# Optimization experiments

Hardware: AMD Instinct MI355X
Metric: run time of the kernel (lower is better)

Reference implementation:

```python
import jax, jax.numpy as jnp
import numpy as np

MAX_POS = 1024  # max_pos_embed_distance
H = 12          # num_heads
D = 768         # input_dim == hidden_dim
P = D // H      # head_dim


def setup_inputs() -> dict:
    key = jax.random.key(0)
    ks = jax.random.split(key, 8)
    s = 1.0 / np.sqrt(D)
    return {
        "x": jax.random.normal(ks[0], (8, 1024, D), dtype=jnp.float32),
        "wq": jax.random.uniform(ks[1], (D, D), jnp.float32, -s, s),
        "bq": jax.random.uniform(ks[2], (D,), jnp.float32, -s, s),
        "wk": jax.random.uniform(ks[3], (D, D), jnp.float32, -s, s),
        "bk": jax.random.uniform(ks[4], (D,), jnp.float32, -s, s),
        "wv": jax.random.uniform(ks[5], (D, D), jnp.float32, -s, s),
        "bv": jax.random.uniform(ks[6], (D,), jnp.float32, -s, s),
        "dist_emb": jax.random.normal(ks[7], (2 * MAX_POS - 1, P), dtype=jnp.float32),
    }


def reference(x, wq, bq, wk, bk, wv, bv, dist_emb):
    b, n, _ = x.shape
    factor = 1.0 / np.sqrt(P)
    # q,k,v: [b, n, h, p]
    q = (x @ wq.T + bq).reshape(b, n, H, P)
    k = (x @ wk.T + bk).reshape(b, n, H, P)
    v = (x @ wv.T + bv).reshape(b, n, H, P)
    raw = jnp.einsum('bihd,bjhd->bhij', q, k)
    # relative-key bias: pos_emb[i, r] = dist_emb[i - r + MAX_POS - 1]
    dist = jnp.arange(n)[:, None] - jnp.arange(n)[None, :]
    pos_emb = dist_emb[dist + MAX_POS - 1]           # [n, n, p]
    raw = raw + jnp.einsum('bihd,ird->bhir', q, pos_emb)
    # NOTE: original scales AFTER adding relative scores
    attn = jax.nn.softmax(raw * factor, axis=-1)
    out = jnp.einsum('bhij,bjhp->bihp', attn, v)
    return out.reshape(b, n, -1)
```

## Files before the change

### kernel.cpp

```cpp
#include <hip/hip_runtime.h>
#include <hip/hip_bf16.h>

#define NH 12
#define HD 64
#define DM 768
#define SEQ 1024
#define BATCH 8

typedef __attribute__((ext_vector_type(8))) short bf16x8;
typedef __attribute__((ext_vector_type(4))) short s16x4;
typedef __attribute__((ext_vector_type(4))) float f32x4;

__device__ __forceinline__ short f2b(float x) {
    unsigned u = __float_as_uint(x);
    u += 0x7fffu + ((u >> 16) & 1u);
    return (short)(u >> 16);
}

#define MFMA(A, B, C) __builtin_amdgcn_mfma_f32_16x16x32_bf16(A, B, C, 0, 0, 0)

__global__ __launch_bounds__(256) void cvt_f32_bf16(
    const float* __restrict__ in, short* __restrict__ out, int n4)
{
    int i = blockIdx.x * 256 + threadIdx.x;
    if (i < n4) {
        f32x4 v = *(const f32x4*)(in + 4 * (size_t)i);
        s16x4 r;
        r[0] = f2b(v[0]); r[1] = f2b(v[1]); r[2] = f2b(v[2]); r[3] = f2b(v[3]);
        *(s16x4*)(out + 4 * (size_t)i) = r;
    }
}

__global__ __launch_bounds__(512, 4) void qkv_mfma(
    const short* __restrict__ xb,
    const short* __restrict__ wqb, const float* __restrict__ bq,
    const short* __restrict__ wkb, const float* __restrict__ bk,
    const short* __restrict__ wvb, const float* __restrict__ bv,
    short* __restrict__ qb, short* __restrict__ kb, short* __restrict__ vt)
{
    __shared__ short Xl[128][72];
    __shared__ short Wl[64][72];

    const int orig = blockIdx.x;
    const int sw   = (orig & 7) * 288 + (orig >> 3);
    const int t    = sw % 36;
    const int by   = t % 12;
    const int z    = t / 12;
    const int bx   = sw / 36;

    const short* wmat = (z == 0) ? wqb : (z == 1) ? wkb : wvb;
    const float* bias = (z == 0) ? bq : (z == 1) ? bk : bv;

    const int i0   = bx * 128;
    const int col0 = by * 64;
    const int tid  = threadIdx.x;
    const int lane = tid & 63;
    const int w    = tid >> 6;
    const int lg   = lane >> 4;
    const int lc   = lane & 15;

    const int sr = tid >> 3, scx = (tid & 7) * 8;

    f32x4 acc[4] = {};
    for (int k0 = 0; k0 < DM; k0 += 64) {
        __syncthreads();
        *(bf16x8*)&Xl[sr][scx] =
            *(const bf16x8*)&xb[(size_t)(i0 + sr) * DM + k0 + scx];
        *(bf16x8*)&Xl[sr + 64][scx] =
            *(const bf16x8*)&xb[(size_t)(i0 + 64 + sr) * DM + k0 + scx];
        *(bf16x8*)&Wl[sr][scx] =
            *(const bf16x8*)&wmat[(size_t)(col0 + sr) * DM + k0 + scx];
        __syncthreads();
        #pragma unroll
        for (int kh = 0; kh < 2; ++kh) {
            const bf16x8 a = *(const bf16x8*)&Xl[w * 16 + lc][kh * 32 + lg * 8];
            #pragma unroll
            for (int n = 0; n < 4; ++n) {
                const bf16x8 bfr = *(const bf16x8*)&Wl[n * 16 + lc][kh * 32 + lg * 8];
                acc[n] = MFMA(a, bfr, acc[n]);
            }
        }
    }

    if (z < 2) {
        short* outp = (z == 0) ? qb : kb;
        #pragma unroll
        for (int n = 0; n < 4; ++n) {
            const int c = col0 + n * 16 + lc;
            const float bi = bias[c];
            #pragma unroll
            for (int rr = 0; rr < 4; ++rr) {
                const int r = i0 + w * 16 + lg * 4 + rr;
                outp[(size_t)r * DM + c] = f2b(acc[n][rr] + bi);
            }
        }
    } else {
        #pragma unroll
        for (int n = 0; n < 4; ++n) {
            const int c = col0 + n * 16 + lc;
            const int h = c >> 6, d = c & 63;
            const float bi = bias[c];
            #pragma unroll
            for (int rr = 0; rr < 4; ++rr) {
                const int r  = i0 + w * 16 + lg * 4 + rr;
                const int bb = r >> 10, j = r & 1023;
                vt[(((size_t)bb * NH + h) * HD + d) * SEQ + j] = f2b(acc[n][rr] + bi);
            }
        }
    }
}

__global__ __launch_bounds__(512, 4) void attn_flash(
    const short* __restrict__ qb, const short* __restrict__ kb,
    const short* __restrict__ vt, const short* __restrict__ deb,
    float* __restrict__ out)
{
    const int orig = blockIdx.x;
    const int sw   = (orig & 7) * 96 + (orig >> 3);
    const int bx   = sw & 7;
    const int rest = sw >> 3;
    const int h    = rest % NH;
    const int b    = rest / NH;

    const int i0   = bx * 128;
    const int tid  = threadIdx.x;
    const int lane = tid & 63;
    const int w    = tid >> 6;
    const int wR   = w * 16;
    const int lg   = lane >> 4;
    const int lc   = lane & 15;

    __shared__ short Kl[64][72];
    __shared__ short Dl[192][72];
    __shared__ short Pl[8][16][136];

    const short* qrow = qb + ((size_t)(b * SEQ + i0 + wR + lc)) * DM + h * HD;
    const bf16x8 A0 = *(const bf16x8*)(qrow + lg * 8);
    const bf16x8 A1 = *(const bf16x8*)(qrow + 32 + lg * 8);

    const short* kbase = kb + (size_t)(b * SEQ) * DM + h * HD;
    const short* vbase = vt + ((size_t)(b * NH + h) * HD) * SEQ;

    const int sr = tid >> 3, scx = (tid & 7) * 8;
    bf16x8 kreg, dreg0, dreg1, dreg2;

    auto stage_load = [&](int jc) {
        kreg = *(const bf16x8*)&kbase[(size_t)(jc + sr) * DM + scx];
        const int wb = i0 - jc + 960;
        const int r2 = min(wb + sr + 128, 2046);
        dreg0 = *(const bf16x8*)&deb[(size_t)(wb + sr) * HD + scx];
        dreg1 = *(const bf16x8*)&deb[(size_t)(wb + sr + 64) * HD + scx];
        dreg2 = *(const bf16x8*)&deb[(size_t)r2 * HD + scx];
    };
    auto stage_store = [&]() {
        *(bf16x8*)&Kl[sr][scx]       = kreg;
        *(bf16x8*)&Dl[sr][scx]       = dreg0;
        *(bf16x8*)&Dl[sr + 64][scx]  = dreg1;
        *(bf16x8*)&Dl[sr + 128][scx] = dreg2;
    };

    float m[4], l[4];
    f32x4 O0 = {0.f,0.f,0.f,0.f}, O1 = {0.f,0.f,0.f,0.f};
    f32x4 O2 = {0.f,0.f,0.f,0.f}, O3 = {0.f,0.f,0.f,0.f};
    #pragma unroll
    for (int rr = 0; rr < 4; ++rr) { m[rr] = -1e30f; l[rr] = 0.f; }

    stage_load(0);
    stage_store();
    __syncthreads();

    for (int c = 0; c < 16; ++c) {
        const int jc = c * 64;
        if (c < 15) stage_load(jc + 64);

        f32x4 T0, T1, T2, T3, T4;
        {
            f32x4 a;
            a = f32x4{0.f,0.f,0.f,0.f};
            a = MFMA(A0, *(const bf16x8*)&Dl[wR + 0*16 + lc][lg*8], a);
            T0 = MFMA(A1, *(const bf16x8*)&Dl[wR + 0*16 + lc][32 + lg*8], a);
            a = f32x4{0.f,0.f,0.f,0.f};
            a = MFMA(A0, *(const bf16x8*)&Dl[wR + 1*16 + lc][lg*8], a);
            T1 = MFMA(A1, *(const bf16x8*)&Dl[wR + 1*16 + lc][32 + lg*8], a);
            a = f32x4{0.f,0.f,0.f,0.f};
            a = MFMA(A0, *(const bf16x8*)&Dl[wR + 2*16 + lc][lg*8], a);
            T2 = MFMA(A1, *(const bf16x8*)&Dl[wR + 2*16 + lc][32 + lg*8], a);
            a = f32x4{0.f,0.f,0.f,0.f};
            a = MFMA(A0, *(const bf16x8*)&Dl[wR + 3*16 + lc][lg*8], a);
            T3 = MFMA(A1, *(const bf16x8*)&Dl[wR + 3*16 + lc][32 + lg*8], a);
            a = f32x4{0.f,0.f,0.f,0.f};
            a = MFMA(A0, *(const bf16x8*)&Dl[wR + 4*16 + lc][lg*8], a);
            T4 = MFMA(A1, *(const bf16x8*)&Dl[wR + 4*16 + lc][32 + lg*8], a);
        }

        f32x4 sv[4];
        #pragma unroll
        for (int jt = 0; jt < 4; ++jt) {
            f32x4 s = {0.f,0.f,0.f,0.f};
            s = MFMA(A0, *(const bf16x8*)&Kl[jt*16 + lc][lg*8], s);
            s = MFMA(A1, *(const bf16x8*)&Kl[jt*16 + lc][32 + lg*8], s);
            sv[jt] = s;
        }
        __syncthreads();

        float mw[4] = {-1e30f, -1e30f, -1e30f, -1e30f};
        #pragma unroll
        for (int jt = 0; jt < 4; ++jt) {
            #pragma unroll
            for (int rr = 0; rr < 4; ++rr) {
                const int loff = 63 + lg * 4 + rr - jt * 16 - lc;
                const int src  = (lane & 48) | (loff & 15);
                float c0, c1;
                if (jt == 0)      { c0 = __shfl(T3[rr], src, 64); c1 = __shfl(T4[rr], src, 64); }
                else if (jt == 1) { c0 = __shfl(T2[rr], src, 64); c1 = __shfl(T3[rr], src, 64); }
                else if (jt == 2) { c0 = __shfl(T1[rr], src, 64); c1 = __shfl(T2[rr], src, 64); }
                else              { c0 = __shfl(T0[rr], src, 64); c1 = __shfl(T1[rr], src, 64); }
                const int tlo = 3 - jt;
                float bias = ((loff >> 4) == tlo) ? c0 : c1;
                sv[jt][rr] += bias;
                mw[rr] = fmaxf(mw[rr], sv[jt][rr]);
            }
        }

        float scale[4];
        #pragma unroll
        for (int rr = 0; rr < 4; ++rr) {
            float v = mw[rr];
            v = fmaxf(v, __shfl_xor(v, 1, 64));
            v = fmaxf(v, __shfl_xor(v, 2, 64));
            v = fmaxf(v, __shfl_xor(v, 4, 64));
            v = fmaxf(v, __shfl_xor(v, 8, 64));
            const float mn = fmaxf(m[rr], v);
            scale[rr] = __expf((m[rr] - mn) * 0.125f);
            m[rr] = mn;
            float s = 0.f;
            #pragma unroll
            for (int jt = 0; jt < 4; ++jt) {
                const float p = __expf((sv[jt][rr] - mn) * 0.125f);
                Pl[w][lg * 4 + rr][jt * 16 + lc] = f2b(p);
                s += p;
            }
            s += __shfl_xor(s, 1, 64);
            s += __shfl_xor(s, 2, 64);
            s += __shfl_xor(s, 4, 64);
            s += __shfl_xor(s, 8, 64);
            l[rr] = l[rr] * scale[rr] + s;
        }

        if (c < 15) stage_store();

        #pragma unroll
        for (int rr = 0; rr < 4; ++rr) {
            O0[rr] *= scale[rr]; O1[rr] *= scale[rr];
            O2[rr] *= scale[rr]; O3[rr] *= scale[rr];
        }
        #pragma unroll
        for (int ks = 0; ks < 2; ++ks) {
            const bf16x8 Af = *(const bf16x8*)&Pl[w][lc][ks * 32 + lg * 8];
            const size_t vo = jc + ks * 32 + lg * 8;
            O0 = MFMA(Af, *(const bf16x8*)&vbase[(size_t)( 0 + lc) * SEQ + vo], O0);
            O1 = MFMA(Af, *(const bf16x8*)&vbase[(size_t)(16 + lc) * SEQ + vo], O1);
            O2 = MFMA(Af, *(const bf16x8*)&vbase[(size_t)(32 + lc) * SEQ + vo], O2);
            O3 = MFMA(Af, *(const bf16x8*)&vbase[(size_t)(48 + lc) * SEQ + vo], O3);
        }
        __syncthreads();
    }

    #pragma unroll
    for (int rr = 0; rr < 4; ++rr) {
        const size_t rowoff = ((size_t)(b * SEQ + i0 + wR + lg * 4 + rr)) * DM + h * HD;
        const float inv = 1.0f / l[rr];
        out[rowoff +  0 + lc] = O0[rr] * inv;
        out[rowoff + 16 + lc] = O1[rr] * inv;
        out[rowoff + 32 + lc] = O2[rr] * inv;
        out[rowoff + 48 + lc] = O3[rr] * inv;
    }
}

extern "C" void kernel_launch(void* const* d_in, const int* in_sizes, int n_in,
                              void* d_out, int out_size, void* d_ws, size_t ws_size,
                              hipStream_t stream) {
    const float* x  = (const float*)d_in[0];
    const float* wq = (const float*)d_in[1];
    const float* bq = (const float*)d_in[2];
    const float* wk = (const float*)d_in[3];
    const float* bk = (const float*)d_in[4];
    const float* wv = (const float*)d_in[5];
    const float* bv = (const float*)d_in[6];
    const float* de = (const float*)d_in[7];
    float* out = (float*)d_out;

    const size_t NX = (size_t)BATCH * SEQ * DM;
    const size_t NW = (size_t)DM * DM;
    const size_t ND = 2047 * HD;
    short* xb  = (short*)d_ws;
    short* wqb = xb  + NX;
    short* wkb = wqb + NW;
    short* wvb = wkb + NW;
    short* deb = wvb + NW;
    short* qbw = deb + ND;
    short* kbw = qbw + NX;
    short* vtw = kbw + NX;

    cvt_f32_bf16<<<(int)((NX / 4 + 255) / 256), 256, 0, stream>>>(x,  xb,  (int)(NX / 4));
    cvt_f32_bf16<<<(int)((NW / 4 + 255) / 256), 256, 0, stream>>>(wq, wqb, (int)(NW / 4));
    cvt_f32_bf16<<<(int)((NW / 4 + 255) / 256), 256, 0, stream>>>(wk, wkb, (int)(NW / 4));
    cvt_f32_bf16<<<(int)((NW / 4 + 255) / 256), 256, 0, stream>>>(wv, wvb, (int)(NW / 4));
    cvt_f32_bf16<<<(int)((ND / 4 + 255) / 256), 256, 0, stream>>>(de, deb, (int)(ND / 4));

    qkv_mfma<<<2304, 512, 0, stream>>>(xb, wqb, bq, wkb, bk, wvb, bv,
                                       qbw, kbw, vtw);
    attn_flash<<<768, 512, 0, stream>>>(qbw, kbw, vtw, deb, out);
}
```

Baseline: 383.4 us.

## Double-buffer LDS tiles in QKV and attention kernels, route bias via LDS

The QKV projection kernel now double-buffers its X/W shared tiles, so each k-step needs one barrier instead of two, and its launch-bounds occupancy hint drops from 4 to 2. The attention kernel double-buffers K tiles and drops the shared distance-embedding tile. Each wave instead reads dist_emb directly from global memory, writes the relative-position products to a per-wave float LDS buffer, and gathers the bias from there instead of using cross-lane shuffles. The P tile is XOR-swizzled to reduce LDS bank conflicts. This removes block barriers and shuffle work, at the cost of more LDS traffic, uncoalesced global loads of dist_emb and possibly lower occupancy.

```diff
diff --git a/kernel.cpp b/kernel.cpp
--- a/kernel.cpp
+++ b/kernel.cpp
@@ -18,6 +18,8 @@
 }
 
 #define MFMA(A, B, C) __builtin_amdgcn_mfma_f32_16x16x32_bf16(A, B, C, 0, 0, 0)
+
+#define PSWZ(row, col) ((col) ^ (((row) & 7) << 3))
 
 __global__ __launch_bounds__(256) void cvt_f32_bf16(
     const float* __restrict__ in, short* __restrict__ out, int n4)
@@ -31,15 +33,15 @@
     }
 }
 
-__global__ __launch_bounds__(512, 4) void qkv_mfma(
+__global__ __launch_bounds__(512, 2) void qkv_mfma(
     const short* __restrict__ xb,
     const short* __restrict__ wqb, const float* __restrict__ bq,
     const short* __restrict__ wkb, const float* __restrict__ bk,
     const short* __restrict__ wvb, const float* __restrict__ bv,
     short* __restrict__ qb, short* __restrict__ kb, short* __restrict__ vt)
 {
-    __shared__ short Xl[128][72];
-    __shared__ short Wl[64][72];
+    __shared__ short Xl[2][128][72];
+    __shared__ short Wl[2][64][72];
 
     const int orig = blockIdx.x;
     const int sw   = (orig & 7) * 288 + (orig >> 3);
@@ -61,25 +63,32 @@
 
     const int sr = tid >> 3, scx = (tid & 7) * 8;
 
+    auto stage = [&](int k0, int buf) {
+        *(bf16x8*)&Xl[buf][sr][scx] =
+            *(const bf16x8*)&xb[(size_t)(i0 + sr) * DM + k0 + scx];
+        *(bf16x8*)&Xl[buf][sr + 64][scx] =
+            *(const bf16x8*)&xb[(size_t)(i0 + 64 + sr) * DM + k0 + scx];
+        *(bf16x8*)&Wl[buf][sr][scx] =
+            *(const bf16x8*)&wmat[(size_t)(col0 + sr) * DM + k0 + scx];
+    };
+
     f32x4 acc[4] = {};
-    for (int k0 = 0; k0 < DM; k0 += 64) {
+    stage(0, 0);
+    __syncthreads();
+
+    for (int ks = 0; ks < 12; ++ks) {
+        const int cur = ks & 1;
+        if (ks < 11) stage((ks + 1) * 64, cur ^ 1);
+        #pragma unroll
+        for (int kh = 0; kh < 2; ++kh) {
+            const bf16x8 a = *(const bf16x8*)&Xl[cur][w * 16 + lc][kh * 32 + lg * 8];
+            #pragma unroll
+            for (int n = 0; n < 4; ++n) {
+                const bf16x8 bfr = *(const bf16x8*)&Wl[cur][n * 16 + lc][kh * 32 + lg * 8];
+                acc[n] = MFMA(a, bfr, acc[n]);
+            }
+        }
         __syncthreads();
-        *(bf16x8*)&Xl[sr][scx] =
-            *(const bf16x8*)&xb[(size_t)(i0 + sr) * DM + k0 + scx];
-        *(bf16x8*)&Xl[sr + 64][scx] =
-            *(const bf16x8*)&xb[(size_t)(i0 + 64 + sr) * DM + k0 + scx];
-        *(bf16x8*)&Wl[sr][scx] =
-            *(const bf16x8*)&wmat[(size_t)(col0 + sr) * DM + k0 + scx];
-        __syncthreads();
-        #pragma unroll
-        for (int kh = 0; kh < 2; ++kh) {
-            const bf16x8 a = *(const bf16x8*)&Xl[w * 16 + lc][kh * 32 + lg * 8];
-            #pragma unroll
-            for (int n = 0; n < 4; ++n) {
-                const bf16x8 bfr = *(const bf16x8*)&Wl[n * 16 + lc][kh * 32 + lg * 8];
-                acc[n] = MFMA(a, bfr, acc[n]);
-            }
-        }
     }
 
     if (z < 2) {
@@ -130,9 +139,9 @@
     const int lg   = lane >> 4;
     const int lc   = lane & 15;
 
-    __shared__ short Kl[64][72];
-    __shared__ short Dl[192][72];
-    __shared__ short Pl[8][16][136];
+    __shared__ short Kl[2][64][72];
+    __shared__ float Tl[8][16][84];
+    __shared__ short Pl[8][16][64];
 
     const short* qrow = qb + ((size_t)(b * SEQ + i0 + wR + lc)) * DM + h * HD;
     const bf16x8 A0 = *(const bf16x8*)(qrow + lg * 8);
@@ -142,21 +151,9 @@
     const short* vbase = vt + ((size_t)(b * NH + h) * HD) * SEQ;
 
     const int sr = tid >> 3, scx = (tid & 7) * 8;
-    bf16x8 kreg, dreg0, dreg1, dreg2;
-
-    auto stage_load = [&](int jc) {
-        kreg = *(const bf16x8*)&kbase[(size_t)(jc + sr) * DM + scx];
-        const int wb = i0 - jc + 960;
-        const int r2 = min(wb + sr + 128, 2046);
-        dreg0 = *(const bf16x8*)&deb[(size_t)(wb + sr) * HD + scx];
-        dreg1 = *(const bf16x8*)&deb[(size_t)(wb + sr + 64) * HD + scx];
-        dreg2 = *(const bf16x8*)&deb[(size_t)r2 * HD + scx];
-    };
-    auto stage_store = [&]() {
-        *(bf16x8*)&Kl[sr][scx]       = kreg;
-        *(bf16x8*)&Dl[sr][scx]       = dreg0;
-        *(bf16x8*)&Dl[sr + 64][scx]  = dreg1;
-        *(bf16x8*)&Dl[sr + 128][scx] = dreg2;
+    auto stage = [&](int jc, int buf) {
+        *(bf16x8*)&Kl[buf][sr][scx] =
+            *(const bf16x8*)&kbase[(size_t)(jc + sr) * DM + scx];
     };
 
     float m[4], l[4];
@@ -165,59 +162,45 @@
     #pragma unroll
     for (int rr = 0; rr < 4; ++rr) { m[rr] = -1e30f; l[rr] = 0.f; }
 
-    stage_load(0);
-    stage_store();
+    stage(0, 0);
     __syncthreads();
 
     for (int c = 0; c < 16; ++c) {
-        const int jc = c * 64;
-        if (c < 15) stage_load(jc + 64);
-
-        f32x4 T0, T1, T2, T3, T4;
-        {
-            f32x4 a;
-            a = f32x4{0.f,0.f,0.f,0.f};
-            a = MFMA(A0, *(const bf16x8*)&Dl[wR + 0*16 + lc][lg*8], a);
-            T0 = MFMA(A1, *(const bf16x8*)&Dl[wR + 0*16 + lc][32 + lg*8], a);
-            a = f32x4{0.f,0.f,0.f,0.f};
-            a = MFMA(A0, *(const bf16x8*)&Dl[wR + 1*16 + lc][lg*8], a);
-            T1 = MFMA(A1, *(const bf16x8*)&Dl[wR + 1*16 + lc][32 + lg*8], a);
-            a = f32x4{0.f,0.f,0.f,0.f};
-            a = MFMA(A0, *(const bf16x8*)&Dl[wR + 2*16 + lc][lg*8], a);
-            T2 = MFMA(A1, *(const bf16x8*)&Dl[wR + 2*16 + lc][32 + lg*8], a);
-            a = f32x4{0.f,0.f,0.f,0.f};
-            a = MFMA(A0, *(const bf16x8*)&Dl[wR + 3*16 + lc][lg*8], a);
-            T3 = MFMA(A1, *(const bf16x8*)&Dl[wR + 3*16 + lc][32 + lg*8], a);
-            a = f32x4{0.f,0.f,0.f,0.f};
-            a = MFMA(A0, *(const bf16x8*)&Dl[wR + 4*16 + lc][lg*8], a);
-            T4 = MFMA(A1, *(const bf16x8*)&Dl[wR + 4*16 + lc][32 + lg*8], a);
+        const int jc  = c * 64;
+        const int cur = c & 1;
+        if (c < 15) stage(jc + 64, cur ^ 1);
+
+        const int wb = i0 + wR - jc + 960;
+        #pragma unroll
+        for (int t = 0; t < 5; ++t) {
+            int drow = wb + t * 16 + lc;
+            if (t == 4) drow = min(drow, 2046);
+            const short* dp = deb + (size_t)drow * HD;
+            f32x4 a = {0.f,0.f,0.f,0.f};
+            a = MFMA(A0, *(const bf16x8*)(dp + lg * 8), a);
+            a = MFMA(A1, *(const bf16x8*)(dp + 32 + lg * 8), a);
+            #pragma unroll
+            for (int rr = 0; rr < 4; ++rr)
+                Tl[w][lg * 4 + rr][t * 16 + lc] = a[rr];
         }
 
         f32x4 sv[4];
         #pragma unroll
         for (int jt = 0; jt < 4; ++jt) {
             f32x4 s = {0.f,0.f,0.f,0.f};
-            s = MFMA(A0, *(const bf16x8*)&Kl[jt*16 + lc][lg*8], s);
-            s = MFMA(A1, *(const bf16x8*)&Kl[jt*16 + lc][32 + lg*8], s);
+            s = MFMA(A0, *(const bf16x8*)&Kl[cur][jt * 16 + lc][lg * 8], s);
+            s = MFMA(A1, *(const bf16x8*)&Kl[cur][jt * 16 + lc][32 + lg * 8], s);
             sv[jt] = s;
         }
-        __syncthreads();
 
         float mw[4] = {-1e30f, -1e30f, -1e30f, -1e30f};
         #pragma unroll
         for (int jt = 0; jt < 4; ++jt) {
             #pragma unroll
             for (int rr = 0; rr < 4; ++rr) {
-                const int loff = 63 + lg * 4 + rr - jt * 16 - lc;
-                const int src  = (lane & 48) | (loff & 15);
-                float c0, c1;
-                if (jt == 0)      { c0 = __shfl(T3[rr], src, 64); c1 = __shfl(T4[rr], src, 64); }
-                else if (jt == 1) { c0 = __shfl(T2[rr], src, 64); c1 = __shfl(T3[rr], src, 64); }
-                else if (jt == 2) { c0 = __shfl(T1[rr], src, 64); c1 = __shfl(T2[rr], src, 64); }
-                else              { c0 = __shfl(T0[rr], src, 64); c1 = __shfl(T1[rr], src, 64); }
-                const int tlo = 3 - jt;
-                float bias = ((loff >> 4) == tlo) ? c0 : c1;
-                sv[jt][rr] += bias;
+                const int row  = lg * 4 + rr;
+                const int loff = 63 + row - jt * 16 - lc;
+                sv[jt][rr] += Tl[w][row][loff];
                 mw[rr] = fmaxf(mw[rr], sv[jt][rr]);
             }
         }
@@ -225,6 +208,7 @@
         float scale[4];
         #pragma unroll
         for (int rr = 0; rr < 4; ++rr) {
+            const int row = lg * 4 + rr;
             float v = mw[rr];
             v = fmaxf(v, __shfl_xor(v, 1, 64));
             v = fmaxf(v, __shfl_xor(v, 2, 64));
@@ -237,7 +221,7 @@
             #pragma unroll
             for (int jt = 0; jt < 4; ++jt) {
                 const float p = __expf((sv[jt][rr] - mn) * 0.125f);
-                Pl[w][lg * 4 + rr][jt * 16 + lc] = f2b(p);
+                Pl[w][row][PSWZ(row, jt * 16 + lc)] = f2b(p);
                 s += p;
             }
             s += __shfl_xor(s, 1, 64);
@@ -247,8 +231,6 @@
             l[rr] = l[rr] * scale[rr] + s;
         }
 
-        if (c < 15) stage_store();
-
         #pragma unroll
         for (int rr = 0; rr < 4; ++rr) {
             O0[rr] *= scale[rr]; O1[rr] *= scale[rr];
@@ -256,7 +238,7 @@
         }
         #pragma unroll
         for (int ks = 0; ks < 2; ++ks) {
-            const bf16x8 Af = *(const bf16x8*)&Pl[w][lc][ks * 32 + lg * 8];
+            const bf16x8 Af = *(const bf16x8*)&Pl[w][lc][PSWZ(lc, ks * 32 + lg * 8)];
             const size_t vo = jc + ks * 32 + lg * 8;
             O0 = MFMA(Af, *(const bf16x8*)&vbase[(size_t)( 0 + lc) * SEQ + vo], O0);
             O1 = MFMA(Af, *(const bf16x8*)&vbase[(size_t)(16 + lc) * SEQ + vo], O1);
```

After: 390.3 us. No clear change (+1.8%).
